# Kernel optimization log

Measured on AMD Instinct MI355X. Metric: run time of the kernel, lower is better.

## Reference

```python
import jax, jax.numpy as jnp
import numpy as np

SIGMA = 1.0
KSIZE = 5
WEAK = 75.0
STRONG = 255.0
LOW_T = 0.00392
HIGH_T = 0.15

# scipy.signal.gaussian(M, std): unnormalized gaussian window
_n = np.arange(KSIZE, dtype=np.float32) - (KSIZE - 1) / 2.0
_g = np.exp(-0.5 * (_n / SIGMA) ** 2).astype(np.float32)
GAUSS_H = jnp.asarray(_g.reshape(1, 1, 1, KSIZE))  # horizontal 1xK
GAUSS_V = jnp.asarray(_g.reshape(1, 1, KSIZE, 1))  # vertical Kx1

_sobel = np.array([[1, 0, -1], [2, 0, -2], [1, 0, -1]], dtype=np.float32)
SOBEL_H = jnp.asarray(_sobel.reshape(1, 1, 3, 3))
SOBEL_V = jnp.asarray(_sobel.T.reshape(1, 1, 3, 3))

_f0 = np.array([[0, 0, 0], [0, 1, -1], [0, 0, 0]], np.float32)
_f45 = np.array([[0, 0, 0], [0, 1, 0], [0, 0, -1]], np.float32)
_f90 = np.array([[0, 0, 0], [0, 1, 0], [0, -1, 0]], np.float32)
_f135 = np.array([[0, 0, 0], [0, 1, 0], [-1, 0, 0]], np.float32)
_f180 = np.array([[0, 0, 0], [-1, 1, 0], [0, 0, 0]], np.float32)
_f225 = np.array([[-1, 0, 0], [0, 1, 0], [0, 0, 0]], np.float32)
_f270 = np.array([[0, -1, 0], [0, 1, 0], [0, 0, 0]], np.float32)
_f315 = np.array([[0, 0, -1], [0, 1, 0], [0, 0, 0]], np.float32)
DIR_FILT = jnp.asarray(np.stack([_f0, _f45, _f90, _f135, _f180, _f225, _f270, _f315]).reshape(8, 1, 3, 3))

NBR_FILT = jnp.asarray(np.array([[1, 1, 1], [1, 0, 1], [1, 1, 1]], np.float32).reshape(1, 1, 3, 3))


def _conv(x, w, pad):
    # cross-correlation, matching torch F.conv2d
    return jax.lax.conv_general_dilated(
        x, w, window_strides=(1, 1), padding=[(pad[0], pad[0]), (pad[1], pad[1])],
        dimension_numbers=('NCHW', 'OIHW', 'NCHW'))


def setup_inputs() -> dict:
    key = jax.random.key(0)
    img = jax.random.uniform(key, (16, 1, 1024, 1024), dtype=jnp.float32)
    return {"img": img}


def reference(img):
    B = img.shape[0]
    # --- gaussian noise removal (separable) ---
    sm = _conv(img, GAUSS_H, (0, KSIZE // 2))
    sm = _conv(sm, GAUSS_V, (KSIZE // 2, 0))
    # --- sobel gradients ---
    Ix = _conv(sm, SOBEL_H, (1, 1))
    Iy = _conv(sm, SOBEL_V, (1, 1))
    mag = jnp.sqrt(Ix ** 2 + Iy ** 2)
    mag = mag / mag.reshape(B, -1).max(axis=1).reshape(B, 1, 1, 1)
    direction = jnp.arctan2(Iy, Ix) * (180.0 / 3.1415926) + 180.0
    direction = jnp.round(direction / 45.0) * 45.0
    # --- non-max suppression via directional differences + gather ---
    all_filtered = _conv(mag, DIR_FILT, (1, 1))  # [B,8,H,W]
    idx_pos = (direction / 45.0).astype(jnp.int32) % 8  # [B,1,H,W]
    idx_neg = (idx_pos + 4) % 8
    cs_pos = jnp.take_along_axis(all_filtered, idx_pos, axis=1)
    cs_neg = jnp.take_along_axis(all_filtered, idx_neg, axis=1)
    is_max = jnp.minimum(cs_pos, cs_neg) > 0.0
    thin = jnp.where(is_max, mag, 0.0)
    # --- double threshold ---
    hi = thin.max() * HIGH_T  # global max, as in source
    strong = thin >= hi
    weak = (thin < hi) & (thin >= LOW_T)
    inter = jnp.where(strong, STRONG, jnp.where(weak, WEAK, 0.0))
    # --- hysteresis: iterate until no weak pixel gains a strong neighbor ---
    def cond(state):
        return state[1]

    def body(state):
        x, _ = state
        weak_m = x == WEAK
        sn = _conv((x == STRONG).astype(jnp.float32), NBR_FILT, (1, 1))
        new_strong = weak_m & (sn > 0.0)
        x = jnp.where(new_strong, STRONG, x)
        return x, new_strong.any()

    final, _ = jax.lax.while_loop(cond, body, (inter, jnp.asarray(True)))
    final = jnp.where(final == STRONG, final, 0.0)
    return final
```

## Files before the change

kernel.cpp:

```cpp
#include <hip/hip_runtime.h>
#include <math.h>

#define BB 16
#define H 1024
#define W 1024
#define HW (H*W)
#define NTOT (BB*HW)

typedef unsigned long long u64;

__device__ __constant__ float GW[5] = {
    0.13533528323661270f, 0.60653065971263342f, 1.0f,
    0.60653065971263342f, 0.13533528323661270f};

#define CSCALE ((float)(180.0 / 3.1415926))

#define TW 128
#define TH 8
__global__ __launch_bounds__(256, 8) void k_smooth_sobel(const float* __restrict__ img,
                                                         float* __restrict__ mag,
                                                         unsigned char* __restrict__ bucket,
                                                         float* __restrict__ partial) {
#pragma clang fp contract(off)
    __shared__ float sA[14 * 136 + 16];
    __shared__ float sB[14 * 132];
    __shared__ float red[256];

    const int tid = threadIdx.x;
    const int x0 = blockIdx.x * TW;
    const int y0 = blockIdx.y * TH;
    const int b = blockIdx.z;
    const size_t base = (size_t)b * HW;

    for (int idx = tid; idx < 14 * 34; idx += 256) {
        int r = idx / 34, v = idx - r * 34;
        int gy = y0 - 3 + r;
        int gxv = x0 - 4 + v * 4;
        float4 val = make_float4(0.f, 0.f, 0.f, 0.f);
        if (gy >= 0 && gy < H && gxv >= 0 && gxv <= W - 4)
            val = *(const float4*)&img[base + (size_t)gy * W + gxv];
        *(float4*)&sA[r * 136 + v * 4] = val;
    }
    __syncthreads();

    for (int idx = tid; idx < 14 * 33; idx += 256) {
        int r = idx / 33, g = idx - r * 33;
        const float* p = &sA[r * 136 + g * 4];
        float4 A0 = *(const float4*)p;
        float4 A1 = *(const float4*)(p + 4);
        float4 A2 = *(const float4*)(p + 8);
        float a_[12] = {A0.x, A0.y, A0.z, A0.w, A1.x, A1.y, A1.z, A1.w,
                        A2.x, A2.y, A2.z, A2.w};
        float o[4];
#pragma unroll
        for (int j = 0; j < 4; ++j) {
            float s = 0.0f;
#pragma unroll
            for (int k = 0; k < 5; ++k) s = s + GW[k] * a_[j + 1 + k];
            o[j] = s;
        }
        *(float4*)&sB[r * 132 + g * 4] = make_float4(o[0], o[1], o[2], o[3]);
    }
    __syncthreads();

    for (int idx = tid; idx < 10 * 33; idx += 256) {
        int rr = idx / 33, g = idx - rr * 33;
        float bb[20];
#pragma unroll
        for (int k = 0; k < 5; ++k) {
            float4 t = *(const float4*)&sB[(rr + k) * 132 + g * 4];
            bb[k * 4 + 0] = t.x; bb[k * 4 + 1] = t.y;
            bb[k * 4 + 2] = t.z; bb[k * 4 + 3] = t.w;
        }
        int gy = y0 - 1 + rr;
        bool rowok = (gy >= 0 && gy < H);
        float o[4];
#pragma unroll
        for (int j = 0; j < 4; ++j) {
            float s = 0.0f;
#pragma unroll
            for (int k = 0; k < 5; ++k) s = s + GW[k] * bb[k * 4 + j];
            int gx = x0 - 1 + g * 4 + j;
            o[j] = (rowok && gx >= 0 && gx < W) ? s : 0.0f;
        }
        *(float4*)&sA[rr * 136 + g * 4] = make_float4(o[0], o[1], o[2], o[3]);
    }
    __syncthreads();

    const int r = tid >> 5;
    const int cg = (tid & 31) * 4;
    const int y = y0 + r;
    const float* P0 = &sA[r * 136 + cg];
    const float* P1 = P0 + 136;
    const float* P2 = P1 + 136;
    float4 q0 = *(const float4*)P0; float2 e0 = *(const float2*)(P0 + 4);
    float4 q1 = *(const float4*)P1; float2 e1 = *(const float2*)(P1 + 4);
    float4 q2 = *(const float4*)P2; float2 e2 = *(const float2*)(P2 + 4);
    float r0[6] = {q0.x, q0.y, q0.z, q0.w, e0.x, e0.y};
    float r1[6] = {q1.x, q1.y, q1.z, q1.w, e1.x, e1.y};
    float r2[6] = {q2.x, q2.y, q2.z, q2.w, e2.x, e2.y};

    float tmax = 0.0f;
    float mg[4];
    unsigned int bk = 0;
#pragma unroll
    for (int j = 0; j < 4; ++j) {
        float a00 = r0[j], a01 = r0[j + 1], a02 = r0[j + 2];
        float a10 = r1[j],                  a12 = r1[j + 2];
        float a20 = r2[j], a21 = r2[j + 1], a22 = r2[j + 2];

        float Ix = a00;
        Ix = Ix - a02;
        Ix = Ix + 2.0f * a10;
        Ix = Ix - 2.0f * a12;
        Ix = Ix + a20;
        Ix = Ix - a22;

        float Iy = a00;
        Iy = Iy + 2.0f * a01;
        Iy = Iy + a02;
        Iy = Iy - a20;
        Iy = Iy - 2.0f * a21;
        Iy = Iy - a22;

        float t1 = Ix * Ix;
        float t2 = Iy * Iy;
        float m = sqrtf(t1 + t2);
        mg[j] = m;
        tmax = fmaxf(tmax, m);

        float ax = fabsf(Ix), ay = fabsf(Iy);
        float mn = fminf(ax, ay), mx = fmaxf(ax, ay);
        float cr = mn * 0.92387953f - mx * 0.38268343f;
        int bidx;
        if (fabsf(cr) < mx * 3e-5f) {
            float fa2 = (float)atan2((double)Iy, (double)Ix);
            float d2 = fa2 * CSCALE;
            d2 = d2 + 180.0f;
            float t2d = d2 / 45.0f;
            float rr2 = rintf(t2d);
            bidx = ((int)rr2) & 7;
        } else if (ay <= ax * 0.41421356f) {
            bidx = signbit(Ix) ? 0 : 4;
        } else if (ay >= ax * 2.41421356f) {
            bidx = (Iy >= 0.0f) ? 6 : 2;
        } else {
            bidx = (Iy >= 0.0f) ? ((Ix >= 0.0f) ? 5 : 7)
                                : ((Ix >= 0.0f) ? 3 : 1);
        }
        bk |= ((unsigned int)bidx) << (8 * j);
    }
    *(float4*)&mag[base + (size_t)y * W + x0 + cg] = make_float4(mg[0], mg[1], mg[2], mg[3]);
    *(unsigned int*)&bucket[base + (size_t)y * W + x0 + cg] = bk;

    red[tid] = tmax;
    __syncthreads();
    for (int s = 128; s > 0; s >>= 1) {
        if (tid < s) red[tid] = fmaxf(red[tid], red[tid + s]);
        __syncthreads();
    }
    if (tid == 0) {
        int pb = (blockIdx.z * 128 + blockIdx.y) * 8 + blockIdx.x;
        partial[pb] = red[0];
    }
}

__global__ __launch_bounds__(256) void k_redmax_img(const float* __restrict__ partial,
                                                    float* __restrict__ magmax) {
    __shared__ float red[256];
    const float* p = partial + blockIdx.x * 1024;
    float m = 0.0f;
    for (int k = threadIdx.x; k < 1024; k += 256) m = fmaxf(m, p[k]);
    red[threadIdx.x] = m;
    __syncthreads();
    for (int s = 128; s > 0; s >>= 1) {
        if (threadIdx.x < s) red[threadIdx.x] = fmaxf(red[threadIdx.x], red[threadIdx.x + s]);
        __syncthreads();
    }
    if (threadIdx.x == 0) magmax[blockIdx.x] = red[0];
}

__global__ __launch_bounds__(256, 8) void k_nms_s(const float* __restrict__ mag,
                                                  const unsigned char* __restrict__ bucket,
                                                  const float* __restrict__ magmax,
                                                  u64* __restrict__ Mb,
                                                  float* __restrict__ partial) {
#pragma clang fp contract(off)
    __shared__ float red[256];
    const int tid = threadIdx.x;
    const int L = tid & 63, wv = tid >> 6;
    const int sx = blockIdx.x * 4 + wv;
    const int x0 = sx * 64;
    const int y0 = blockIdx.y * 64;
    const int b = blockIdx.z;
    const size_t base = (size_t)b * HW;
    const float M = magmax[b];
    const int x = x0 + L;
    const int wbase = (((b << 8) | (blockIdx.y << 4) | sx)) * 64;

    auto loadRow = [&](int y, float& Lv, float& Cv, float& Rv) {
        float c = 0.0f, l = 0.0f, rr = 0.0f;
        if (y >= 0 && y < H) {
            c = mag[base + (size_t)y * W + x];
            l = __shfl_up(c, 1);
            rr = __shfl_down(c, 1);
            if (L == 0)  l = (x0 > 0) ? mag[base + (size_t)y * W + (x0 - 1)] : 0.0f;
            if (L == 63) rr = (x0 + 64 < W) ? mag[base + (size_t)y * W + (x0 + 64)] : 0.0f;
        }
        Lv = l; Cv = c; Rv = rr;
    };

    float pL, pC, pR, cL, cC, cR, nL, nC, nR, fL, fC, fR;
    loadRow(y0 - 1, pL, pC, pR);
    loadRow(y0, cL, cC, cR);
    loadRow(y0 + 1, nL, nC, nR);

    float amax = 0.0f;
    for (int i = 0; i < 64; ++i) {
        int y = y0 + i;
        loadRow(y + 2, fL, fC, fR);
        int bkt = bucket[base + (size_t)y * W + x];
        int t1 = (bkt + 1) & 7;
        bool dyp = (bkt >= 1 && bkt <= 3);
        bool dyn = (bkt >= 5);
        bool dxp = (t1 <= 2);
        bool dxn = (t1 >= 4 && t1 <= 6);

        float rLv = dyn ? pL : (dyp ? nL : cL);
        float rCv = dyn ? pC : (dyp ? nC : cC);
        float rRv = dyn ? pR : (dyp ? nR : cR);
        float bp = dxn ? rLv : (dxp ? rRv : rCv);
        float sLv = dyn ? nL : (dyp ? pL : cL);
        float sCv = dyn ? nC : (dyp ? pC : cC);
        float sRv = dyn ? nR : (dyp ? pR : cR);
        float bn = dxn ? sRv : (dxp ? sLv : sCv);

        float a = cC;
        bool g1 = a > bp, g2 = a > bn;
        bool f1 = a >= bp * 1.0000005f;
        bool f2 = a >= bn * 1.0000005f;
        bool im = g1 && g2;
        bool bad = (g1 && !f1) || (g2 && !f2);
        if (__any(bad)) {
            if (bad) {
                float qa = a / M;
                bool r1 = g1, r2 = g2;
                if (g1 && !f1) r1 = qa > (bp / M);
                if (g2 && !f2) r2 = qa > (bn / M);
                im = r1 && r2;
            }
        }
        if (im) amax = fmaxf(amax, a);
        u64 word = __ballot(im);
        if (L == 0) Mb[wbase + i] = word;

        pL = cL; pC = cC; pR = cR;
        cL = nL; cC = nC; cR = nR;
        nL = fL; nC = fC; nR = fR;
    }

    red[tid] = amax;
    __syncthreads();
    for (int s = 128; s > 0; s >>= 1) {
        if (tid < s) red[tid] = fmaxf(red[tid], red[tid + s]);
        __syncthreads();
    }
    if (tid == 0)
        partial[(blockIdx.z * 16 + blockIdx.y) * 4 + blockIdx.x] = red[0] / M;
}

__global__ __launch_bounds__(1024) void k_finalize_thr(const float* __restrict__ partial,
                                                       float* __restrict__ hdr,
                                                       float* __restrict__ thr) {
    __shared__ float red[1024];
    float m = (threadIdx.x < 1024) ? partial[threadIdx.x] : 0.0f;
    red[threadIdx.x] = m;
    __syncthreads();
    for (int s = 512; s > 0; s >>= 1) {
        if (threadIdx.x < s) red[threadIdx.x] = fmaxf(red[threadIdx.x], red[threadIdx.x + s]);
        __syncthreads();
    }
    if (threadIdx.x == 0) hdr[16] = red[0];
    if (threadIdx.x < 32) {
        float tm = red[0];
        int t = threadIdx.x;
        float M = hdr[t >> 1];
        float T = (t & 1) ? (tm * 0.15f) : 0.00392f;
        if (0.0f / M >= T) { thr[t] = 0.0f; return; }
        unsigned int lo = 0u, hi = 0x7f800000u;
        while (hi - lo > 1u) {
            unsigned int mid = lo + ((hi - lo) >> 1);
            if (__uint_as_float(mid) / M >= T) hi = mid; else lo = mid;
        }
        thr[t] = __uint_as_float(hi);
    }
}

__global__ __launch_bounds__(256, 8) void k_thresh_s(const float* __restrict__ mag,
                                                     const u64* __restrict__ Mb,
                                                     const float* __restrict__ hdr,
                                                     const float* __restrict__ thr,
                                                     u64* __restrict__ Sb,
                                                     u64* __restrict__ Wb) {
    const int tid = threadIdx.x;
    const int L = tid & 63, wv = tid >> 6;
    const int sx = blockIdx.x * 4 + wv;
    const int x0 = sx * 64;
    const int y0 = blockIdx.y * 64;
    const int b = blockIdx.z;
    const size_t base = (size_t)b * HW;
    const float Alo = thr[b * 2], Ahi = thr[b * 2 + 1];
    const bool snm = (hdr[16] * 0.15f <= 0.0f);
    const int wbase = (((b << 8) | (blockIdx.y << 4) | sx)) * 64;

    float a_nxt = mag[base + (size_t)y0 * W + x0 + L];
    u64 mw_nxt = Mb[wbase];
    for (int i = 0; i < 64; ++i) {
        float a = a_nxt;
        u64 mw = mw_nxt;
        if (i < 63) {
            a_nxt = mag[base + (size_t)(y0 + i + 1) * W + x0 + L];
            mw_nxt = Mb[wbase + i + 1];
        }
        bool im = (mw >> L) & 1ull;
        bool strong = snm || (im && (a >= Ahi));
        bool weak = (!strong) && im && (a >= Alo);
        u64 sw = __ballot(strong);
        u64 ww = __ballot(weak);
        if (L == 0) { Sb[wbase + i] = sw; Wb[wbase + i] = ww; }
    }
}

template <bool LAST>
__global__ __launch_bounds__(256) void k_hyster_bits(const u64* __restrict__ Wb,
                                                     u64* __restrict__ Sb,
                                                     float* __restrict__ out) {
    const int lane = threadIdx.x & 63;
    const int t = blockIdx.x * 4 + (threadIdx.x >> 6);
    const int ty = (t >> 4) & 15;
    const int tx = t & 15;
    const int idx = t * 64 + lane;

    u64 S = Sb[idx];
    const u64 Wk = Wb[idx];

    u64 hstat = 0;
    if (tx > 0)  hstat |= (Sb[(t - 1) * 64 + lane] >> 63) & 1ull;
    if (tx < 15) hstat |= (Sb[(t + 1) * 64 + lane] & 1ull) << 63;

    u64 halo = 0;
    if (lane == 0 && ty > 0) {
        const int ta = t - 16;
        u64 tc = Sb[ta * 64 + 63];
        u64 hh = (tc << 1) | tc | (tc >> 1);
        if (tx > 0)  hh |= (Sb[(ta - 1) * 64 + 63] >> 63) & 1ull;
        if (tx < 15) hh |= (Sb[(ta + 1) * 64 + 63] & 1ull) << 63;
        halo = hh;
    }
    if (lane == 63 && ty < 15) {
        const int tb = t + 16;
        u64 tc = Sb[tb * 64 + 0];
        u64 hh = (tc << 1) | tc | (tc >> 1);
        if (tx > 0)  hh |= (Sb[(tb - 1) * 64 + 0] >> 63) & 1ull;
        if (tx < 15) hh |= (Sb[(tb + 1) * 64 + 0] & 1ull) << 63;
        halo = hh;
    }

    for (int it = 0; it < 160; ++it) {
        u64 hh = (S << 1) | S | (S >> 1) | hstat;
        u64 up = __shfl_up(hh, 1, 64);
        if (lane == 0) up = halo;
        u64 dn = __shfl_down(hh, 1, 64);
        if (lane == 63) dn = halo;
        u64 dil = hh | up | dn;
        u64 nS = S | (Wk & dil);
        bool ch = (nS != S);
        S = nS;
        if (!__any(ch)) break;
    }

    if (!LAST) {
        Sb[idx] = S;
    } else {
        const int bimg = t >> 8;
        float* op = out + (size_t)bimg * HW + (size_t)(ty * 64) * W + tx * 64 + lane;
#pragma unroll 4
        for (int rr = 0; rr < 64; ++rr) {
            u64 wrow = __shfl(S, rr, 64);
            op[(size_t)rr * W] = ((wrow >> lane) & 1ull) ? 255.0f : 0.0f;
        }
    }
}

extern "C" void kernel_launch(void* const* d_in, const int* in_sizes, int n_in,
                              void* d_out, int out_size, void* d_ws, size_t ws_size,
                              hipStream_t stream) {
    (void)in_sizes; (void)n_in; (void)out_size; (void)ws_size;
    const float* img = (const float*)d_in[0];
    float* out = (float*)d_out;

    float* hdr = (float*)d_ws;
    float* thr = hdr + 64;
    float* partialA = hdr + 128;
    float* partialB = partialA + 16384;
    float* A = partialB + 4096;
    unsigned char* C = (unsigned char*)(A + (size_t)NTOT);
    u64* Sb = (u64*)(C + (size_t)NTOT);
    u64* Wb = Sb + NTOT / 64;
    u64* Mb = Wb + NTOT / 64;

    dim3 blk(256);
    k_smooth_sobel<<<dim3(8, 128, BB), blk, 0, stream>>>(img, A, C, partialA);
    k_redmax_img<<<dim3(BB), blk, 0, stream>>>(partialA, hdr);
    k_nms_s<<<dim3(4, 16, BB), blk, 0, stream>>>(A, C, hdr, Mb, partialB);
    k_finalize_thr<<<dim3(1), dim3(1024), 0, stream>>>(partialB, hdr, thr);
    k_thresh_s<<<dim3(4, 16, BB), blk, 0, stream>>>(A, Mb, hdr, thr, Sb, Wb);
    for (int p = 0; p < 5; ++p)
        k_hyster_bits<false><<<dim3(NTOT / (64 * 64) / 4), blk, 0, stream>>>(Wb, Sb, out);
    k_hyster_bits<true><<<dim3(NTOT / (64 * 64) / 4), blk, 0, stream>>>(Wb, Sb, out);
}
```

Baseline: 293.3 us.

## Retile NMS and threshold kernels into 128x32 blocks with LDS-staged magnitude

The non-max suppression kernel now stages a 34x136 halo tile of the magnitude in shared memory with float4 loads. It then looks up the two directional neighbours by computed offset instead of shuffling rows through registers. Both NMS and threshold kernels switch from 64-row column strips to 128x32 tiles, which gives four times as many blocks for more parallelism, and the partial-max reduction is widened to match. The trade is extra LDS traffic, a block-wide sync, and some halo reloading.

```diff
diff --git a/kernel.cpp b/kernel.cpp
--- a/kernel.cpp
+++ b/kernel.cpp
@@ -180,62 +180,54 @@
     if (threadIdx.x == 0) magmax[blockIdx.x] = red[0];
 }
 
-__global__ __launch_bounds__(256, 8) void k_nms_s(const float* __restrict__ mag,
-                                                  const unsigned char* __restrict__ bucket,
-                                                  const float* __restrict__ magmax,
-                                                  u64* __restrict__ Mb,
-                                                  float* __restrict__ partial) {
+__global__ __launch_bounds__(256, 8) void k_nms_b2(const float* __restrict__ mag,
+                                                   const unsigned char* __restrict__ bucket,
+                                                   const float* __restrict__ magmax,
+                                                   u64* __restrict__ Mb,
+                                                   float* __restrict__ partial) {
 #pragma clang fp contract(off)
+    __shared__ float sN[34 * 136];
     __shared__ float red[256];
+
     const int tid = threadIdx.x;
-    const int L = tid & 63, wv = tid >> 6;
-    const int sx = blockIdx.x * 4 + wv;
-    const int x0 = sx * 64;
-    const int y0 = blockIdx.y * 64;
+    const int x0 = blockIdx.x * 128;
+    const int y0 = blockIdx.y * 32;
     const int b = blockIdx.z;
     const size_t base = (size_t)b * HW;
     const float M = magmax[b];
-    const int x = x0 + L;
-    const int wbase = (((b << 8) | (blockIdx.y << 4) | sx)) * 64;
-
-    auto loadRow = [&](int y, float& Lv, float& Cv, float& Rv) {
-        float c = 0.0f, l = 0.0f, rr = 0.0f;
-        if (y >= 0 && y < H) {
-            c = mag[base + (size_t)y * W + x];
-            l = __shfl_up(c, 1);
-            rr = __shfl_down(c, 1);
-            if (L == 0)  l = (x0 > 0) ? mag[base + (size_t)y * W + (x0 - 1)] : 0.0f;
-            if (L == 63) rr = (x0 + 64 < W) ? mag[base + (size_t)y * W + (x0 + 64)] : 0.0f;
-        }
-        Lv = l; Cv = c; Rv = rr;
-    };
-
-    float pL, pC, pR, cL, cC, cR, nL, nC, nR, fL, fC, fR;
-    loadRow(y0 - 1, pL, pC, pR);
-    loadRow(y0, cL, cC, cR);
-    loadRow(y0 + 1, nL, nC, nR);
-
+
+    for (int idx = tid; idx < 34 * 34; idx += 256) {
+        int r = idx / 34, v = idx - r * 34;
+        int gy = y0 - 1 + r;
+        int gxv = x0 - 4 + v * 4;
+        float4 val = make_float4(0.f, 0.f, 0.f, 0.f);
+        if (gy >= 0 && gy < H && gxv >= 0 && gxv <= W - 4)
+            val = *(const float4*)&mag[base + (size_t)gy * W + gxv];
+        *(float4*)&sN[r * 136 + v * 4] = val;
+    }
+    __syncthreads();
+
+    const int L = tid & 63, wv = tid >> 6;
+    const int h = wv & 1, wr = wv >> 1;
+    const int c = h * 64 + L;
+    const int txw = (x0 >> 6) + h;
     float amax = 0.0f;
-    for (int i = 0; i < 64; ++i) {
-        int y = y0 + i;
-        loadRow(y + 2, fL, fC, fR);
-        int bkt = bucket[base + (size_t)y * W + x];
+
+#pragma unroll 4
+    for (int i = 0; i < 16; ++i) {
+        const int r = i * 2 + wr;
+        const int y = y0 + r;
+        int bkt = bucket[base + (size_t)y * W + x0 + c];
         int t1 = (bkt + 1) & 7;
-        bool dyp = (bkt >= 1 && bkt <= 3);
-        bool dyn = (bkt >= 5);
-        bool dxp = (t1 <= 2);
-        bool dxn = (t1 >= 4 && t1 <= 6);
-
-        float rLv = dyn ? pL : (dyp ? nL : cL);
-        float rCv = dyn ? pC : (dyp ? nC : cC);
-        float rRv = dyn ? pR : (dyp ? nR : cR);
-        float bp = dxn ? rLv : (dxp ? rRv : rCv);
-        float sLv = dyn ? nL : (dyp ? pL : cL);
-        float sCv = dyn ? nC : (dyp ? pC : cC);
-        float sRv = dyn ? nR : (dyp ? pR : cR);
-        float bn = dxn ? sRv : (dxp ? sLv : sCv);
-
-        float a = cC;
+        int dy = ((bkt >= 1 && bkt <= 3) ? 1 : 0) - ((bkt >= 5) ? 1 : 0);
+        int dx = ((t1 <= 2) ? 1 : 0) - ((t1 >= 4 && t1 <= 6) ? 1 : 0);
+
+        const int o = (r + 1) * 136 + c + 4;
+        const int od = dy * 136 + dx;
+        float a  = sN[o];
+        float bp = sN[o + od];
+        float bn = sN[o - od];
+
         bool g1 = a > bp, g2 = a > bn;
         bool f1 = a >= bp * 1.0000005f;
         bool f2 = a >= bn * 1.0000005f;
@@ -252,11 +244,7 @@
         }
         if (im) amax = fmaxf(amax, a);
         u64 word = __ballot(im);
-        if (L == 0) Mb[wbase + i] = word;
-
-        pL = cL; pC = cC; pR = cR;
-        cL = nL; cC = nC; cR = nR;
-        nL = fL; nC = fC; nR = fR;
+        if (L == 0) Mb[((b << 8) | ((y >> 6) << 4) | txw) * 64 + (y & 63)] = word;
     }
 
     red[tid] = amax;
@@ -266,14 +254,15 @@
         __syncthreads();
     }
     if (tid == 0)
-        partial[(blockIdx.z * 16 + blockIdx.y) * 4 + blockIdx.x] = red[0] / M;
+        partial[(blockIdx.z * 32 + blockIdx.y) * 8 + blockIdx.x] = red[0] / M;
 }
 
 __global__ __launch_bounds__(1024) void k_finalize_thr(const float* __restrict__ partial,
                                                        float* __restrict__ hdr,
                                                        float* __restrict__ thr) {
     __shared__ float red[1024];
-    float m = (threadIdx.x < 1024) ? partial[threadIdx.x] : 0.0f;
+    float m = 0.0f;
+    for (int k = threadIdx.x; k < 4096; k += 1024) m = fmaxf(m, partial[k]);
     red[threadIdx.x] = m;
     __syncthreads();
     for (int s = 512; s > 0; s >>= 1) {
@@ -296,7 +285,7 @@
     }
 }
 
-__global__ __launch_bounds__(256, 8) void k_thresh_s(const float* __restrict__ mag,
+__global__ __launch_bounds__(256, 8) void k_thresh_w(const float* __restrict__ mag,
                                                      const u64* __restrict__ Mb,
                                                      const float* __restrict__ hdr,
                                                      const float* __restrict__ thr,
@@ -304,30 +293,28 @@
                                                      u64* __restrict__ Wb) {
     const int tid = threadIdx.x;
     const int L = tid & 63, wv = tid >> 6;
-    const int sx = blockIdx.x * 4 + wv;
-    const int x0 = sx * 64;
-    const int y0 = blockIdx.y * 64;
+    const int h = wv & 1, wr = wv >> 1;
+    const int x0 = blockIdx.x * 128;
+    const int y0 = blockIdx.y * 32;
     const int b = blockIdx.z;
     const size_t base = (size_t)b * HW;
     const float Alo = thr[b * 2], Ahi = thr[b * 2 + 1];
     const bool snm = (hdr[16] * 0.15f <= 0.0f);
-    const int wbase = (((b << 8) | (blockIdx.y << 4) | sx)) * 64;
-
-    float a_nxt = mag[base + (size_t)y0 * W + x0 + L];
-    u64 mw_nxt = Mb[wbase];
-    for (int i = 0; i < 64; ++i) {
-        float a = a_nxt;
-        u64 mw = mw_nxt;
-        if (i < 63) {
-            a_nxt = mag[base + (size_t)(y0 + i + 1) * W + x0 + L];
-            mw_nxt = Mb[wbase + i + 1];
-        }
+    const int txw = (x0 >> 6) + h;
+
+#pragma unroll 4
+    for (int i = 0; i < 16; ++i) {
+        const int r = i * 2 + wr;
+        const int y = y0 + r;
+        const int widx = ((b << 8) | ((y >> 6) << 4) | txw) * 64 + (y & 63);
+        float a = mag[base + (size_t)y * W + x0 + h * 64 + L];
+        u64 mw = Mb[widx];
         bool im = (mw >> L) & 1ull;
         bool strong = snm || (im && (a >= Ahi));
         bool weak = (!strong) && im && (a >= Alo);
         u64 sw = __ballot(strong);
         u64 ww = __ballot(weak);
-        if (L == 0) { Sb[wbase + i] = sw; Wb[wbase + i] = ww; }
+        if (L == 0) { Sb[widx] = sw; Wb[widx] = ww; }
     }
 }
 
@@ -412,9 +399,9 @@
     dim3 blk(256);
     k_smooth_sobel<<<dim3(8, 128, BB), blk, 0, stream>>>(img, A, C, partialA);
     k_redmax_img<<<dim3(BB), blk, 0, stream>>>(partialA, hdr);
-    k_nms_s<<<dim3(4, 16, BB), blk, 0, stream>>>(A, C, hdr, Mb, partialB);
+    k_nms_b2<<<dim3(8, 32, BB), blk, 0, stream>>>(A, C, hdr, Mb, partialB);
     k_finalize_thr<<<dim3(1), dim3(1024), 0, stream>>>(partialB, hdr, thr);
-    k_thresh_s<<<dim3(4, 16, BB), blk, 0, stream>>>(A, Mb, hdr, thr, Sb, Wb);
+    k_thresh_w<<<dim3(8, 32, BB), blk, 0, stream>>>(A, Mb, hdr, thr, Sb, Wb);
     for (int p = 0; p < 5; ++p)
         k_hyster_bits<false><<<dim3(NTOT / (64 * 64) / 4), blk, 0, stream>>>(Wb, Sb, out);
     k_hyster_bits<true><<<dim3(NTOT / (64 * 64) / 4), blk, 0, stream>>>(Wb, Sb, out);
```

After: 257.4 us. 1.14x faster.
